# Kernel tuning notes

Hardware: AMD Instinct MI355X
Metric: run time of the kernel (lower is better)

Reference implementation:

```python
import jax, jax.numpy as jnp
import numpy as np

N_SRC = 50000
N_DST = 50000
E = 640000
D_IN = 128
D_OUT = 128
H = 4
D_HEAD = D_OUT // H


def setup_inputs() -> dict:
    key = jax.random.key(0)
    k1, k2, k3, k4, k5, k6 = jax.random.split(key, 6)
    src_feat = jax.random.normal(k1, (N_SRC, D_IN), dtype=jnp.float32)
    dst_feat = jax.random.normal(k2, (N_DST, D_IN), dtype=jnp.float32)
    src_idx = jax.random.randint(k3, (E,), 0, N_SRC)
    dst_idx = jax.random.randint(k4, (E,), 0, N_DST)
    edge_index = jnp.stack([src_idx, dst_idx], axis=0)  # [2, E]
    # nn.Linear(d_in, d_out, bias=False): store as [d_in, d_out] so h = x @ W
    W = jax.random.normal(k5, (D_IN, D_OUT), dtype=jnp.float32) * (1.0 / np.sqrt(D_IN))
    # nn.Linear(2*d_head, 1, bias=False): attention vector of length 2*d_head
    a = jax.random.normal(k6, (2 * D_HEAD,), dtype=jnp.float32) * (1.0 / np.sqrt(2 * D_HEAD))
    return {"src_feat": src_feat, "dst_feat": dst_feat, "edge_index": edge_index,
            "W": W, "a": a, "num_dst": N_DST}


def reference(src_feat, dst_feat, edge_index, W, a, num_dst):
    # Dropout in eval mode (identity).
    d_out = W.shape[1]
    d_head = d_out // H
    src_idx = edge_index[0]
    dst_idx = edge_index[1]

    h_src = (src_feat @ W).reshape(-1, H, d_head)  # [N_src, H, d_head]
    h_dst = (dst_feat @ W).reshape(-1, H, d_head)  # [N_dst, H, d_head]
    h_src_e = h_src[src_idx]                        # [E, H, d_head]
    h_dst_e = h_dst[dst_idx]                        # [E, H, d_head]

    # a^T [h_src || h_dst] == h_src . a_src + h_dst . a_dst (shared across heads)
    a_src, a_dst = a[:d_head], a[d_head:]
    e = jax.nn.elu(jnp.einsum('ehd,d->eh', h_src_e, a_src)
                   + jnp.einsum('ehd,d->eh', h_dst_e, a_dst))  # [E, H]

    # Segment softmax over edges grouped by destination node.
    e_max = jax.ops.segment_max(e, dst_idx, num_segments=num_dst)      # [N_dst, H]
    exp_e = jnp.exp(e - e_max[dst_idx])
    denom = jax.ops.segment_sum(exp_e, dst_idx, num_segments=num_dst)  # [N_dst, H]
    alpha = exp_e / (denom[dst_idx] + 1e-12)                           # [E, H]

    # Scatter-add of weighted messages.
    out = jax.ops.segment_sum(alpha[..., None] * h_src_e, dst_idx,
                              num_segments=num_dst)                    # [N_dst, H, d_head]
    return out.reshape(num_dst, d_out)
```

## Files before the change

kernel.cpp:

```cpp
#include <hip/hip_runtime.h>
#include <math.h>

constexpr int N_SRC_ = 50000;
constexpr int N_DST_ = 50000;
constexpr int N_TOT_ = 100000;
constexpr int E_     = 640000;
constexpr int D_     = 128;
constexpr int CAP_   = 64;
constexpr int NTILE  = (N_SRC_ + 31) / 32;
constexpr int MMB    = (NTILE + 3) / 4;
constexpr int SCB    = E_ / 256;

typedef float f32x4  __attribute__((ext_vector_type(4)));
typedef short bf16x8 __attribute__((ext_vector_type(8)));

union U4 { unsigned int u[4]; bf16x8 v; };

static __device__ __forceinline__ unsigned short f2bf_rne(float f) {
    unsigned int x = __float_as_uint(f);
    return (unsigned short)((x + 0x7FFFu + ((x >> 16) & 1u)) >> 16);
}

__global__ __launch_bounds__(256) void k_prep(
    const float* __restrict__ W, const float* __restrict__ a,
    unsigned short* __restrict__ wt, float* __restrict__ va)
{
    int tid = blockIdx.x * 256 + threadIdx.x;
    if (tid >= 136 * 16) return;
    int n = tid >> 4, c = tid & 15;
    if (n < 128) {
        int slot = c ^ (n & 15);
        size_t base = (size_t)n * 128 + slot * 8;
#pragma unroll
        for (int j = 0; j < 8; ++j) {
            int k = c * 8 + j;
            wt[base + j] = f2bf_rne(W[(size_t)k * 128 + n]);
        }
    } else {
        int col = n - 128, half = col >> 2, hd = col & 3;
#pragma unroll
        for (int j = 0; j < 8; ++j) {
            int k = c * 8 + j;
            float acc = 0.f;
            for (int c2 = 0; c2 < 32; ++c2)
                acc += W[(size_t)k * 128 + hd * 32 + c2] * a[half * 32 + c2];
            va[(size_t)k * 8 + col] = acc;
        }
    }
}

__global__ __launch_bounds__(256) void k_s2(
    const float* __restrict__ src, const float* __restrict__ dst,
    const float* __restrict__ va, float* __restrict__ s)
{
    __shared__ float vl[128 * 8];
    __shared__ float al[32 * 132];
    const int t = threadIdx.x;

    ((float4*)vl)[t] = ((const float4*)va)[t];

    const int base = blockIdx.x * 32;
#pragma unroll
    for (int i = 0; i < 4; ++i) {
        int q = t + 256 * i;
        int row = q >> 5, c4 = q & 31;
        int gr = base + row;
        float4 v = make_float4(0.f, 0.f, 0.f, 0.f);
        if (gr < N_TOT_) {
            const float* p = (gr < N_SRC_) ? (src + (size_t)gr * D_)
                                           : (dst + (size_t)(gr - N_SRC_) * D_);
            v = ((const float4*)p)[c4];
        }
        *(float4*)&al[row * 132 + c4 * 4] = v;
    }
    __syncthreads();

    const int node = t >> 3, part = t & 7;
    const int gr = base + node;
    const int half = (gr >= N_SRC_) ? 1 : 0;
    float a0 = 0.f, a1 = 0.f, a2 = 0.f, a3 = 0.f;
#pragma unroll
    for (int kk = 0; kk < 16; ++kk) {
        int k = part * 16 + kk;
        float fv = al[node * 132 + k];
        const float* vp = &vl[k * 8 + half * 4];
        a0 = fmaf(fv, vp[0], a0);
        a1 = fmaf(fv, vp[1], a1);
        a2 = fmaf(fv, vp[2], a2);
        a3 = fmaf(fv, vp[3], a3);
    }
    a0 += __shfl_xor(a0, 1, 64); a0 += __shfl_xor(a0, 2, 64); a0 += __shfl_xor(a0, 4, 64);
    a1 += __shfl_xor(a1, 1, 64); a1 += __shfl_xor(a1, 2, 64); a1 += __shfl_xor(a1, 4, 64);
    a2 += __shfl_xor(a2, 1, 64); a2 += __shfl_xor(a2, 2, 64); a2 += __shfl_xor(a2, 4, 64);
    a3 += __shfl_xor(a3, 1, 64); a3 += __shfl_xor(a3, 2, 64); a3 += __shfl_xor(a3, 4, 64);
    if (part == 0 && gr < N_TOT_)
        *(float4*)&s[(size_t)gr * 4] = make_float4(a0, a1, a2, a3);
}

__global__ __launch_bounds__(256) void k_mms(
    const float* __restrict__ src, const unsigned short* __restrict__ wt,
    const int* __restrict__ src_idx, const int* __restrict__ dst_idx,
    const float* __restrict__ s,
    int* __restrict__ cursor, int* __restrict__ bucket_sn,
    uint2* __restrict__ bucket_w, unsigned int* __restrict__ h)
{
    if (blockIdx.x >= MMB) {
        int e = (int)(blockIdx.x - MMB) * 256 + threadIdx.x;
        int sn = src_idx[e], dn = dst_idx[e];
        float4 vs = *(const float4*)&s[(size_t)sn * 4];
        float4 vd = *(const float4*)&s[(size_t)(N_SRC_ + dn) * 4];
        float x[4] = {vs.x + vd.x, vs.y + vd.y, vs.z + vd.z, vs.w + vd.w};
        float w[4];
#pragma unroll
        for (int hd = 0; hd < 4; ++hd) {
            float eh = x[hd] > 0.f ? x[hd] : (__expf(x[hd]) - 1.f);
            w[hd] = __expf(eh);
        }
        uint2 p;
        p.x = (unsigned int)f2bf_rne(w[0]) | ((unsigned int)f2bf_rne(w[1]) << 16);
        p.y = (unsigned int)f2bf_rne(w[2]) | ((unsigned int)f2bf_rne(w[3]) << 16);
        int pos = atomicAdd(&cursor[dn], 1);
        if (pos < CAP_) {
            bucket_sn[(size_t)dn * CAP_ + pos] = sn;
            bucket_w[(size_t)dn * CAP_ + pos] = p;
        }
        return;
    }

    __shared__ unsigned short wl[128 * 128];
    const int t = threadIdx.x;
    {
        const float4* gw = (const float4*)wt;
        float4* sw = (float4*)wl;
#pragma unroll
        for (int i = 0; i < 8; ++i) sw[t + 256 * i] = gw[t + 256 * i];
    }
    __syncthreads();

    const int wid = t >> 6, lane = t & 63;
    const int g = lane >> 4, sidx = lane & 15;
    const int wtile = blockIdx.x * 4 + wid;
    if (wtile >= NTILE) return;
    const int base = wtile * 32;
    const int r0 = base + sidx;
    const int r1g = base + 16 + sidx;
    const int r1 = (r1g < N_SRC_) ? r1g : 0;
    const float* p0 = src + (size_t)r0 * D_;
    const float* p1 = src + (size_t)r1 * D_;

    f32x4 acc[2][8];
#pragma unroll
    for (int m = 0; m < 2; ++m)
#pragma unroll
        for (int nf = 0; nf < 8; ++nf) acc[m][nf] = (f32x4)0.f;

#pragma unroll
    for (int ks = 0; ks < 4; ++ks) {
        const int k0 = ks * 32 + g * 8;
        bf16x8 af[2];
#pragma unroll
        for (int m = 0; m < 2; ++m) {
            const float* p = m ? p1 : p0;
            float4 v0 = *(const float4*)(p + k0);
            float4 v1 = *(const float4*)(p + k0 + 4);
            float f[8] = {v0.x, v0.y, v0.z, v0.w, v1.x, v1.y, v1.z, v1.w};
            U4 P;
#pragma unroll
            for (int q = 0; q < 4; ++q)
                P.u[q] = (unsigned int)f2bf_rne(f[2 * q])
                       | ((unsigned int)f2bf_rne(f[2 * q + 1]) << 16);
            af[m] = P.v;
        }
#pragma unroll
        for (int nf = 0; nf < 8; ++nf) {
            const int n = nf * 16 + sidx;
            const int off = n * 128 + ((ks * 4 + g) ^ sidx) * 8;
            bf16x8 b = *(const bf16x8*)&wl[off];
            acc[0][nf] = __builtin_amdgcn_mfma_f32_16x16x32_bf16(af[0], b, acc[0][nf], 0, 0, 0);
            acc[1][nf] = __builtin_amdgcn_mfma_f32_16x16x32_bf16(af[1], b, acc[1][nf], 0, 0, 0);
        }
    }

#pragma unroll
    for (int m = 0; m < 2; ++m) {
        const int rowb = base + m * 16 + g * 4;
#pragma unroll
        for (int r = 0; r < 4; ++r) {
            const int row = rowb + r;
            if (row < N_SRC_) {
#pragma unroll
                for (int q = 0; q < 4; ++q) {
                    unsigned int val = (unsigned int)f2bf_rne(acc[m][2 * q][r])
                                     | ((unsigned int)f2bf_rne(acc[m][2 * q + 1][r]) << 16);
                    h[(size_t)row * 64 + q * 16 + sidx] = val;
                }
            }
        }
    }
}

__global__ __launch_bounds__(256) void k_gather(
    const unsigned int* __restrict__ h2, const int* __restrict__ cursor,
    const int* __restrict__ bucket_sn, const uint2* __restrict__ bucket_w,
    float* __restrict__ out)
{
    int wid = (blockIdx.x * 256 + threadIdx.x) >> 6;
    int lane = threadIdx.x & 63;
    if (wid >= N_DST_) return;
    int cnt = min(cursor[wid], CAP_);
    const int hd = lane >> 4;
    const int sub = lane & 15;

    int bval = (lane < cnt) ? bucket_sn[(size_t)wid * CAP_ + lane] : 0;

    float2 acc = make_float2(0.f, 0.f);
    float den = 0.f;
#pragma unroll
    for (int i = 0; i < CAP_; ++i) {
        if (i >= cnt) break;
        int sn = __shfl(bval, i, 64);
        uint2 bw = bucket_w[(size_t)wid * CAP_ + i];
        unsigned int uw = (hd & 2) ? bw.y : bw.x;
        float w = __uint_as_float((hd & 1) ? (uw & 0xFFFF0000u) : (uw << 16));
        den += w;
        unsigned int v = h2[(size_t)sn * 64 + lane];
        acc.x = fmaf(w, __uint_as_float(v << 16), acc.x);
        acc.y = fmaf(w, __uint_as_float(v & 0xFFFF0000u), acc.y);
    }

    float inv = 1.f / (den + 1e-12f);
    out[(size_t)wid * D_ + 32 * hd + sub]      = acc.x * inv;
    out[(size_t)wid * D_ + 32 * hd + sub + 16] = acc.y * inv;
}

extern "C" void kernel_launch(void* const* d_in, const int* in_sizes, int n_in,
                              void* d_out, int out_size, void* d_ws, size_t ws_size,
                              hipStream_t stream)
{
    const float* src_feat = (const float*)d_in[0];
    const float* dst_feat = (const float*)d_in[1];
    const int*   edge     = (const int*)d_in[2];
    const int*   src_idx  = edge;
    const int*   dst_idx  = edge + E_;
    const float* W        = (const float*)d_in[3];
    const float* a        = (const float*)d_in[4];
    float*       out      = (float*)d_out;

    char* p = (char*)d_ws;
    auto alloc = [&](size_t bytes) {
        char* r = p;
        p += (bytes + 255) & ~(size_t)255;
        return r;
    };
    unsigned int* h       = (unsigned int*)alloc((size_t)N_SRC_ * 64 * 4);
    float*  s             = (float*)alloc((size_t)N_TOT_ * 4 * sizeof(float));
    int*    cursor        = (int*)alloc((size_t)N_DST_ * sizeof(int));
    int*    bucket_sn     = (int*)alloc((size_t)N_DST_ * CAP_ * sizeof(int));
    uint2*  bucket_w      = (uint2*)alloc((size_t)N_DST_ * CAP_ * sizeof(uint2));
    unsigned short* wt    = (unsigned short*)alloc((size_t)128 * 128 * 2);
    float*  va            = (float*)alloc((size_t)128 * 8 * sizeof(float));

    hipMemsetAsync(cursor, 0, (size_t)N_DST_ * sizeof(int), stream);

    k_prep<<<(136 * 16 + 255) / 256, 256, 0, stream>>>(W, a, wt, va);
    k_s2<<<(N_TOT_ + 31) / 32, 256, 0, stream>>>(src_feat, dst_feat, va, s);
    k_mms<<<MMB + SCB, 256, 0, stream>>>(src_feat, wt, src_idx, dst_idx, s,
                                         cursor, bucket_sn, bucket_w, h);
    k_gather<<<(N_DST_ * 64 + 255) / 256, 256, 0, stream>>>(
        h, cursor, bucket_sn, bucket_w, out);
}
```

Before: 216.2 us.

## Pack bucket entries, partition scatter by dst range, restructure score and gather kernels

Rewrites the score kernel as a grid-stride, one-wave-per-two-nodes dot product that reads feature rows directly instead of staging them in shared memory. The edge scatter now packs the source index and bf16 weights into a single 16-byte entry, and has each block pass over a 2048-edge chunk handling only edges whose destination falls into one of 8 ranges. This is meant to keep the atomic and bucket-write footprint of concurrent blocks localized in cache. The gather kernel reads the packed entries with one vector load and unrolls by 4 with independent accumulators to raise memory-level parallelism. The costs are that dst_idx is read 8 times, the bucket array grows to 16 bytes per slot with padding, and summation order changes.

```diff
diff --git a/kernel.cpp b/kernel.cpp
--- a/kernel.cpp
+++ b/kernel.cpp
@@ -9,7 +9,9 @@
 constexpr int CAP_   = 64;
 constexpr int NTILE  = (N_SRC_ + 31) / 32;
 constexpr int MMB    = (NTILE + 3) / 4;
-constexpr int SCB    = E_ / 256;
+constexpr int NCHUNK = (E_ + 2047) / 2048;
+constexpr int SCB    = NCHUNK * 8;
+constexpr int DPR    = N_DST_ / 8;
 
 typedef float f32x4  __attribute__((ext_vector_type(4)));
 typedef short bf16x8 __attribute__((ext_vector_type(8)));
@@ -53,76 +55,77 @@
     const float* __restrict__ src, const float* __restrict__ dst,
     const float* __restrict__ va, float* __restrict__ s)
 {
-    __shared__ float vl[128 * 8];
-    __shared__ float al[32 * 132];
-    const int t = threadIdx.x;
-
-    ((float4*)vl)[t] = ((const float4*)va)[t];
-
-    const int base = blockIdx.x * 32;
-#pragma unroll
-    for (int i = 0; i < 4; ++i) {
-        int q = t + 256 * i;
-        int row = q >> 5, c4 = q & 31;
-        int gr = base + row;
-        float4 v = make_float4(0.f, 0.f, 0.f, 0.f);
-        if (gr < N_TOT_) {
-            const float* p = (gr < N_SRC_) ? (src + (size_t)gr * D_)
-                                           : (dst + (size_t)(gr - N_SRC_) * D_);
-            v = ((const float4*)p)[c4];
-        }
-        *(float4*)&al[row * 132 + c4 * 4] = v;
-    }
-    __syncthreads();
-
-    const int node = t >> 3, part = t & 7;
-    const int gr = base + node;
-    const int half = (gr >= N_SRC_) ? 1 : 0;
-    float a0 = 0.f, a1 = 0.f, a2 = 0.f, a3 = 0.f;
-#pragma unroll
-    for (int kk = 0; kk < 16; ++kk) {
-        int k = part * 16 + kk;
-        float fv = al[node * 132 + k];
-        const float* vp = &vl[k * 8 + half * 4];
-        a0 = fmaf(fv, vp[0], a0);
-        a1 = fmaf(fv, vp[1], a1);
-        a2 = fmaf(fv, vp[2], a2);
-        a3 = fmaf(fv, vp[3], a3);
-    }
-    a0 += __shfl_xor(a0, 1, 64); a0 += __shfl_xor(a0, 2, 64); a0 += __shfl_xor(a0, 4, 64);
-    a1 += __shfl_xor(a1, 1, 64); a1 += __shfl_xor(a1, 2, 64); a1 += __shfl_xor(a1, 4, 64);
-    a2 += __shfl_xor(a2, 1, 64); a2 += __shfl_xor(a2, 2, 64); a2 += __shfl_xor(a2, 4, 64);
-    a3 += __shfl_xor(a3, 1, 64); a3 += __shfl_xor(a3, 2, 64); a3 += __shfl_xor(a3, 4, 64);
-    if (part == 0 && gr < N_TOT_)
-        *(float4*)&s[(size_t)gr * 4] = make_float4(a0, a1, a2, a3);
+    const int gw = (blockIdx.x * 256 + threadIdx.x) >> 6;
+    const int lane = threadIdx.x & 63;
+    const int l32 = lane & 31, hf = lane >> 5;
+
+    float4 vs[4], vd[4];
+#pragma unroll
+    for (int j = 0; j < 4; ++j) {
+        const float* vp = va + (size_t)(4 * l32 + j) * 8;
+        vs[j] = *(const float4*)vp;
+        vd[j] = *(const float4*)(vp + 4);
+    }
+
+    for (int p = gw; p < N_TOT_ / 2; p += 2048) {
+        int node = p * 2 + hf;
+        bool is_src = node < N_SRC_;
+        const float* f = is_src ? src + (size_t)node * D_
+                                : dst + (size_t)(node - N_SRC_) * D_;
+        float4 x = *(const float4*)(f + l32 * 4);
+        float4 v0 = is_src ? vs[0] : vd[0];
+        float4 v1 = is_src ? vs[1] : vd[1];
+        float4 v2 = is_src ? vs[2] : vd[2];
+        float4 v3 = is_src ? vs[3] : vd[3];
+        float a0 = x.x * v0.x + x.y * v1.x + x.z * v2.x + x.w * v3.x;
+        float a1 = x.x * v0.y + x.y * v1.y + x.z * v2.y + x.w * v3.y;
+        float a2 = x.x * v0.z + x.y * v1.z + x.z * v2.z + x.w * v3.z;
+        float a3 = x.x * v0.w + x.y * v1.w + x.z * v2.w + x.w * v3.w;
+#pragma unroll
+        for (int m = 1; m < 32; m <<= 1) {
+            a0 += __shfl_xor(a0, m, 64);
+            a1 += __shfl_xor(a1, m, 64);
+            a2 += __shfl_xor(a2, m, 64);
+            a3 += __shfl_xor(a3, m, 64);
+        }
+        if (l32 == 0)
+            *(float4*)&s[(size_t)node * 4] = make_float4(a0, a1, a2, a3);
+    }
 }
 
 __global__ __launch_bounds__(256) void k_mms(
     const float* __restrict__ src, const unsigned short* __restrict__ wt,
     const int* __restrict__ src_idx, const int* __restrict__ dst_idx,
     const float* __restrict__ s,
-    int* __restrict__ cursor, int* __restrict__ bucket_sn,
-    uint2* __restrict__ bucket_w, unsigned int* __restrict__ h)
+    int* __restrict__ cursor, uint4* __restrict__ bucket,
+    unsigned int* __restrict__ h)
 {
     if (blockIdx.x >= MMB) {
-        int e = (int)(blockIdx.x - MMB) * 256 + threadIdx.x;
-        int sn = src_idx[e], dn = dst_idx[e];
-        float4 vs = *(const float4*)&s[(size_t)sn * 4];
-        float4 vd = *(const float4*)&s[(size_t)(N_SRC_ + dn) * 4];
-        float x[4] = {vs.x + vd.x, vs.y + vd.y, vs.z + vd.z, vs.w + vd.w};
-        float w[4];
-#pragma unroll
-        for (int hd = 0; hd < 4; ++hd) {
-            float eh = x[hd] > 0.f ? x[hd] : (__expf(x[hd]) - 1.f);
-            w[hd] = __expf(eh);
-        }
-        uint2 p;
-        p.x = (unsigned int)f2bf_rne(w[0]) | ((unsigned int)f2bf_rne(w[1]) << 16);
-        p.y = (unsigned int)f2bf_rne(w[2]) | ((unsigned int)f2bf_rne(w[3]) << 16);
-        int pos = atomicAdd(&cursor[dn], 1);
-        if (pos < CAP_) {
-            bucket_sn[(size_t)dn * CAP_ + pos] = sn;
-            bucket_w[(size_t)dn * CAP_ + pos] = p;
+        int bid = (int)blockIdx.x - MMB;
+        int r = bid & 7;
+        int ebase = (bid >> 3) * 2048 + threadIdx.x;
+#pragma unroll
+        for (int ii = 0; ii < 8; ++ii) {
+            int e = ebase + ii * 256;
+            if (e >= E_) break;
+            int dn = dst_idx[e];
+            if (dn / DPR != r) continue;
+            int sn = src_idx[e];
+            float4 vsv = *(const float4*)&s[(size_t)sn * 4];
+            float4 vdv = *(const float4*)&s[(size_t)(N_SRC_ + dn) * 4];
+            float x0 = vsv.x + vdv.x, x1 = vsv.y + vdv.y;
+            float x2 = vsv.z + vdv.z, x3 = vsv.w + vdv.w;
+            float w0 = __expf(x0 > 0.f ? x0 : (__expf(x0) - 1.f));
+            float w1 = __expf(x1 > 0.f ? x1 : (__expf(x1) - 1.f));
+            float w2 = __expf(x2 > 0.f ? x2 : (__expf(x2) - 1.f));
+            float w3 = __expf(x3 > 0.f ? x3 : (__expf(x3) - 1.f));
+            uint4 ent;
+            ent.x = (unsigned int)sn;
+            ent.y = (unsigned int)f2bf_rne(w0) | ((unsigned int)f2bf_rne(w1) << 16);
+            ent.z = (unsigned int)f2bf_rne(w2) | ((unsigned int)f2bf_rne(w3) << 16);
+            ent.w = 0u;
+            int pos = atomicAdd(&cursor[dn], 1);
+            if (pos < CAP_) bucket[(size_t)dn * CAP_ + pos] = ent;
         }
         return;
     }
@@ -201,8 +204,7 @@
 
 __global__ __launch_bounds__(256) void k_gather(
     const unsigned int* __restrict__ h2, const int* __restrict__ cursor,
-    const int* __restrict__ bucket_sn, const uint2* __restrict__ bucket_w,
-    float* __restrict__ out)
+    const uint4* __restrict__ bucket, float* __restrict__ out)
 {
     int wid = (blockIdx.x * 256 + threadIdx.x) >> 6;
     int lane = threadIdx.x & 63;
@@ -210,24 +212,45 @@
     int cnt = min(cursor[wid], CAP_);
     const int hd = lane >> 4;
     const int sub = lane & 15;
-
-    int bval = (lane < cnt) ? bucket_sn[(size_t)wid * CAP_ + lane] : 0;
-
-    float2 acc = make_float2(0.f, 0.f);
-    float den = 0.f;
-#pragma unroll
-    for (int i = 0; i < CAP_; ++i) {
-        if (i >= cnt) break;
-        int sn = __shfl(bval, i, 64);
-        uint2 bw = bucket_w[(size_t)wid * CAP_ + i];
-        unsigned int uw = (hd & 2) ? bw.y : bw.x;
-        float w = __uint_as_float((hd & 1) ? (uw & 0xFFFF0000u) : (uw << 16));
-        den += w;
-        unsigned int v = h2[(size_t)sn * 64 + lane];
-        acc.x = fmaf(w, __uint_as_float(v << 16), acc.x);
-        acc.y = fmaf(w, __uint_as_float(v & 0xFFFF0000u), acc.y);
-    }
-
+    const uint4* B = bucket + (size_t)wid * CAP_;
+
+    auto wext = [&](const uint4& e) {
+        unsigned int u = (hd & 2) ? e.z : e.y;
+        return __uint_as_float((hd & 1) ? (u & 0xFFFF0000u) : (u << 16));
+    };
+
+    float2 A0 = make_float2(0.f, 0.f), A1 = A0, A2 = A0, A3 = A0;
+    float d0 = 0.f, d1 = 0.f, d2 = 0.f, d3 = 0.f;
+    int i = 0;
+    for (; i + 4 <= cnt; i += 4) {
+        uint4 e0 = B[i], e1 = B[i + 1], e2 = B[i + 2], e3 = B[i + 3];
+        unsigned int v0 = h2[(size_t)e0.x * 64 + lane];
+        unsigned int v1 = h2[(size_t)e1.x * 64 + lane];
+        unsigned int v2 = h2[(size_t)e2.x * 64 + lane];
+        unsigned int v3 = h2[(size_t)e3.x * 64 + lane];
+        float w0 = wext(e0), w1 = wext(e1), w2 = wext(e2), w3 = wext(e3);
+        d0 += w0; d1 += w1; d2 += w2; d3 += w3;
+        A0.x = fmaf(w0, __uint_as_float(v0 << 16), A0.x);
+        A0.y = fmaf(w0, __uint_as_float(v0 & 0xFFFF0000u), A0.y);
+        A1.x = fmaf(w1, __uint_as_float(v1 << 16), A1.x);
+        A1.y = fmaf(w1, __uint_as_float(v1 & 0xFFFF0000u), A1.y);
+        A2.x = fmaf(w2, __uint_as_float(v2 << 16), A2.x);
+        A2.y = fmaf(w2, __uint_as_float(v2 & 0xFFFF0000u), A2.y);
+        A3.x = fmaf(w3, __uint_as_float(v3 << 16), A3.x);
+        A3.y = fmaf(w3, __uint_as_float(v3 & 0xFFFF0000u), A3.y);
+    }
+    for (; i < cnt; ++i) {
+        uint4 e = B[i];
+        unsigned int v = h2[(size_t)e.x * 64 + lane];
+        float w = wext(e);
+        d0 += w;
+        A0.x = fmaf(w, __uint_as_float(v << 16), A0.x);
+        A0.y = fmaf(w, __uint_as_float(v & 0xFFFF0000u), A0.y);
+    }
+
+    float den = (d0 + d1) + (d2 + d3);
+    float2 acc = make_float2((A0.x + A1.x) + (A2.x + A3.x),
+                             (A0.y + A1.y) + (A2.y + A3.y));
     float inv = 1.f / (den + 1e-12f);
     out[(size_t)wid * D_ + 32 * hd + sub]      = acc.x * inv;
     out[(size_t)wid * D_ + 32 * hd + sub + 16] = acc.y * inv;
@@ -252,20 +275,19 @@
         p += (bytes + 255) & ~(size_t)255;
         return r;
     };
-    unsigned int* h       = (unsigned int*)alloc((size_t)N_SRC_ * 64 * 4);
-    float*  s             = (float*)alloc((size_t)N_TOT_ * 4 * sizeof(float));
-    int*    cursor        = (int*)alloc((size_t)N_DST_ * sizeof(int));
-    int*    bucket_sn     = (int*)alloc((size_t)N_DST_ * CAP_ * sizeof(int));
-    uint2*  bucket_w      = (uint2*)alloc((size_t)N_DST_ * CAP_ * sizeof(uint2));
-    unsigned short* wt    = (unsigned short*)alloc((size_t)128 * 128 * 2);
-    float*  va            = (float*)alloc((size_t)128 * 8 * sizeof(float));
+    unsigned int* h    = (unsigned int*)alloc((size_t)N_SRC_ * 64 * 4);
+    float*  s          = (float*)alloc((size_t)N_TOT_ * 4 * sizeof(float));
+    int*    cursor     = (int*)alloc((size_t)N_DST_ * sizeof(int));
+    uint4*  bucket     = (uint4*)alloc((size_t)N_DST_ * CAP_ * sizeof(uint4));
+    unsigned short* wt = (unsigned short*)alloc((size_t)128 * 128 * 2);
+    float*  va         = (float*)alloc((size_t)128 * 8 * sizeof(float));
 
     hipMemsetAsync(cursor, 0, (size_t)N_DST_ * sizeof(int), stream);
 
     k_prep<<<(136 * 16 + 255) / 256, 256, 0, stream>>>(W, a, wt, va);
-    k_s2<<<(N_TOT_ + 31) / 32, 256, 0, stream>>>(src_feat, dst_feat, va, s);
+    k_s2<<<512, 256, 0, stream>>>(src_feat, dst_feat, va, s);
     k_mms<<<MMB + SCB, 256, 0, stream>>>(src_feat, wt, src_idx, dst_idx, s,
-                                         cursor, bucket_sn, bucket_w, h);
+                                         cursor, bucket, h);
     k_gather<<<(N_DST_ * 64 + 255) / 256, 256, 0, stream>>>(
-        h, cursor, bucket_sn, bucket_w, out);
-}
+        h, cursor, bucket, out);
+}
```

Measured after the change: 216.7 us. About the same (+0.3%).
